# Kernel tuning notes

Measured on AMD Instinct MI355X. Metric: run time of the kernel, lower is better.

Reference implementation:

```python
import jax, jax.numpy as jnp
import numpy as np

N_BATCH = 4096
D_FEAT = 64
N_CLASSES = 10
DET_EPS = 1e-8


def setup_inputs() -> dict:
    key = jax.random.key(0)
    k1, k2, k3 = jax.random.split(key, 3)
    # small-magnitude means and variances bounded away from 0 keep the
    # KL values (and hence sigmoid(KL)) in a numerically meaningful range
    mu = jax.random.normal(k1, (N_BATCH, D_FEAT), dtype=jnp.float32) * 0.1
    var = jax.random.uniform(k2, (N_BATCH, D_FEAT), dtype=jnp.float32) + 0.5
    labels = jax.random.randint(k3, (N_BATCH,), 0, N_CLASSES)
    return {"mu": mu, "var": var, "labels": labels}


def _pairwise_kl(mu, var):
    """K[i, j] = KL(N(mu_i, diag(var_i)) || N(mu_j, diag(var_j))),
    matching the original's kl_mvn on the row/col tiling, but computed
    elementwise/matmul instead of dense diag_embed + inv/det (same math:
    inv(diag(S1)) @ diag(S0) summed == sum(S0/S1); det(diag(S)) == prod(S))."""
    D = mu.shape[1]
    inv_var = 1.0 / var                                   # [N, D]
    # tr term: sum_d var_i,d / var_j,d
    tr = var @ inv_var.T                                  # [N, N]
    # det term: det(S1)/ (det(S0)+eps) with diagonal determinants = products
    p = jnp.prod(var, axis=1)                             # [N]
    det = p[None, :] / (p[:, None] + DET_EPS)             # [N, N]
    # quad term: sum_d (mu_j - mu_i)^2 / var_j,d, expanded into matmuls
    mu_sq = mu * mu                                       # [N, D]
    quad = (mu_sq @ inv_var.T
            - 2.0 * (mu @ (mu * inv_var).T)
            + jnp.sum(mu_sq * inv_var, axis=1)[None, :])  # [N, N]
    return 0.5 * (tr + det + quad - D)


def reference(mu, var, labels):
    N = mu.shape[0]
    K = _pairwise_kl(mu, var)                 # KL(i -> j)
    sym = 0.5 * (K + K.T)                     # symmetric_kl over the pair grid
    logits = jax.nn.sigmoid(sym)              # [N, N]

    same = labels[:, None] == labels[None, :]
    off_diag = ~jnp.eye(N, dtype=bool)        # logits_mask: zero out diagonal
    p_mask = (same & off_diag).astype(logits.dtype)
    n_mask = ((~same) & off_diag).astype(logits.dtype)

    pos = logits * p_mask
    neg = logits * n_mask
    return (jnp.mean(pos), jnp.mean(neg), jnp.sum(pos), jnp.sum(neg))
```

## Files before the change

### kernel.cpp

```cpp
#include <hip/hip_runtime.h>


#define N 4096
#define D 64
#define KH 256
#define MT 128
#define TILES2 32
#define NBLK2 528
#define DET_EPS 1e-8f

typedef short bf16x8 __attribute__((ext_vector_type(8)));
typedef float f32x16 __attribute__((ext_vector_type(16)));

#define WS_H    0
#define WS_PSL  (N * KH * 2)
#define WS_PART (WS_PSL + N * 16)
#define WS_CNT  (WS_PART + 2 * NBLK2 * 4)

static __device__ __forceinline__ unsigned short f2bf(float x) {
  unsigned int u = __float_as_uint(x);
  unsigned int r = (u + 0x7FFFu + ((u >> 16) & 1u)) >> 16;
  return (unsigned short)r;
}

static __device__ __forceinline__ f32x16 mfma_bf16(bf16x8 a, bf16x8 b, f32x16 c) {
  return __builtin_amdgcn_mfma_f32_32x32x16_bf16(a, b, c, 0, 0, 0);
}

__global__ __launch_bounds__(256) void precompute_kernel(
    const float* __restrict__ mu, const float* __restrict__ var,
    const int* __restrict__ labels,
    unsigned short* __restrict__ Hf, float4* __restrict__ PSL,
    int* __restrict__ counter) {
  const int t = threadIdx.x;
  const int lane = t & 63;
  const int w = t >> 6;
  const int r = blockIdx.x * 4 + w;

  if (blockIdx.x == 0 && t == 0) *counter = 0;

  const float m = mu[r * D + lane];
  const float v = var[r * D + lane];
  const float g0 = 1.0f / v;
  const float f0 = v + m * m;
  const float f1 = -2.0f * m;
  const float g1 = m * g0;

  const size_t base = (size_t)(r >> 5) * 8192 + (size_t)(lane >> 2) * 512
                      + (size_t)(r & 31) * 16 + (size_t)(lane & 3) * 4;
  *(ushort4*)&Hf[base] = make_ushort4(f2bf(f0), f2bf(f1), f2bf(g0), f2bf(g1));

  float p = v;
  float s = m * m * g0;
  #pragma unroll
  for (int off = 1; off < 64; off <<= 1) {
    p *= __shfl_xor(p, off);
    s += __shfl_xor(s, off);
  }
  if (lane == 0) {
    PSL[r] = make_float4(p, 1.0f / (p + DET_EPS), 0.25f * s - 16.0f,
                         (float)labels[r]);
  }
}

__global__ __launch_bounds__(256, 2) void pair_kernel(
    const unsigned short* __restrict__ Hf,
    const float4* __restrict__ PSL, float* __restrict__ partial,
    int* __restrict__ counter, float* __restrict__ out) {
  __shared__ float4 sPi[128];
  __shared__ float4 sPj[128];
  __shared__ float red[8];
  __shared__ int lastFlag;
  __shared__ float redp[4], redn[4];

  int L = (int)blockIdx.x;
  int it = (int)(32.5f - sqrtf(32.5f * 32.5f - 2.0f * (float)L));
  while (it > 0 && L < it * TILES2 - it * (it - 1) / 2) --it;
  while (L >= (it + 1) * TILES2 - (it + 1) * it / 2) ++it;
  const int jt = it + (L - (it * TILES2 - it * (it - 1) / 2));
  const int i0 = it * MT, j0 = jt * MT;

  const int t = threadIdx.x;
  const int lane = t & 63;
  const int w = t >> 6;
  const int sr = w >> 1, sc = w & 1;

  if (t < 128) sPi[t] = PSL[i0 + t];
  else sPj[t - 128] = PSL[j0 + t - 128];
  __syncthreads();

  const int l31 = lane & 31;
  const int slot = l31 * 16 + (lane >> 5) * 8;
  const unsigned short* pa = Hf + (size_t)(i0 / 32 + sr * 2) * 8192 + slot;
  const unsigned short* pb = Hf + (size_t)(j0 / 32 + sc * 2) * 8192 + slot;

  const bool active = !(it == jt && w == 2);

  f32x16 C00 = {}, C01 = {}, C10 = {}, C11 = {};
  float pos = 0.0f, neg = 0.0f;

  if (active) {
    #pragma unroll 4
    for (int k = 0; k < 16; ++k) {
      const bf16x8 a0 = *(const bf16x8*)(pa + k * 512);
      const bf16x8 a1 = *(const bf16x8*)(pa + 8192 + k * 512);
      const bf16x8 c0 = *(const bf16x8*)(pb + k * 512);
      const bf16x8 c1 = *(const bf16x8*)(pb + 8192 + k * 512);
      const bf16x8 b0 = __builtin_shufflevector(c0, c0, 2, 3, 0, 1, 6, 7, 4, 5);
      const bf16x8 b1 = __builtin_shufflevector(c1, c1, 2, 3, 0, 1, 6, 7, 4, 5);
      C00 = mfma_bf16(a0, b0, C00);
      C01 = mfma_bf16(a0, b1, C01);
      C10 = mfma_bf16(a1, b0, C10);
      C11 = mfma_bf16(a1, b1, C11);
    }

    const int rbase = 4 * (lane >> 5);
    #pragma unroll
    for (int mn = 0; mn < 4; ++mn) {
      const int m = mn >> 1, n = mn & 1;
      const f32x16 C = (mn == 0) ? C00 : (mn == 1) ? C01 : (mn == 2) ? C10 : C11;
      const int jloc = (sc * 2 + n) * 32 + l31;
      const int j = j0 + jloc;
      const float4 pj = sPj[jloc];
      #pragma unroll
      for (int r = 0; r < 16; ++r) {
        const int row = (r & 3) + 8 * (r >> 2) + rbase;
        const int iloc = (sr * 2 + m) * 32 + row;
        const int i = i0 + iloc;
        if (i < j) {
          const float4 pi = sPi[iloc];
          const float det = pj.x * pi.y + pi.x * pj.y;
          const float sym = 0.25f * (C[r] + det) + pi.z + pj.z;
          const float sig = __builtin_amdgcn_rcpf(1.0f + __expf(-sym));
          if (pi.w == pj.w) pos += sig; else neg += sig;
        }
      }
    }
  }

  #pragma unroll
  for (int off = 32; off > 0; off >>= 1) {
    pos += __shfl_down(pos, off);
    neg += __shfl_down(neg, off);
  }
  if (lane == 0) { red[w] = pos; red[4 + w] = neg; }
  __syncthreads();
  if (t == 0) {
    partial[L]         = red[0] + red[1] + red[2] + red[3];
    partial[NBLK2 + L] = red[4] + red[5] + red[6] + red[7];
    __threadfence();
    const int old = __hip_atomic_fetch_add(counter, 1, __ATOMIC_ACQ_REL,
                                           __HIP_MEMORY_SCOPE_AGENT);
    lastFlag = (old == NBLK2 - 1);
  }
  __syncthreads();

  if (lastFlag) {
    float p = 0.0f, n = 0.0f;
    for (int i = t; i < NBLK2; i += 256) {
      p += __hip_atomic_load(&partial[i], __ATOMIC_RELAXED,
                             __HIP_MEMORY_SCOPE_AGENT);
      n += __hip_atomic_load(&partial[NBLK2 + i], __ATOMIC_RELAXED,
                             __HIP_MEMORY_SCOPE_AGENT);
    }
    #pragma unroll
    for (int off = 32; off > 0; off >>= 1) {
      p += __shfl_down(p, off);
      n += __shfl_down(n, off);
    }
    if (lane == 0) { redp[w] = p; redn[w] = n; }
    __syncthreads();
    if (t == 0) {
      const float posS = 2.0f * (redp[0] + redp[1] + redp[2] + redp[3]);
      const float negS = 2.0f * (redn[0] + redn[1] + redn[2] + redn[3]);
      out[0] = posS * (1.0f / 16777216.0f);
      out[1] = negS * (1.0f / 16777216.0f);
      out[2] = posS;
      out[3] = negS;
    }
  }
}

extern "C" void kernel_launch(void* const* d_in, const int* in_sizes, int n_in,
                              void* d_out, int out_size, void* d_ws, size_t ws_size,
                              hipStream_t stream) {
  const float* mu = (const float*)d_in[0];
  const float* var = (const float*)d_in[1];
  const int* labels = (const int*)d_in[2];
  float* out = (float*)d_out;
  char* ws = (char*)d_ws;

  unsigned short* Hf = (unsigned short*)(ws + WS_H);
  float4* PSL = (float4*)(ws + WS_PSL);
  float* partial = (float*)(ws + WS_PART);
  int* counter = (int*)(ws + WS_CNT);

  precompute_kernel<<<dim3(N / 4), dim3(256), 0, stream>>>(mu, var, labels, Hf,
                                                           PSL, counter);
  pair_kernel<<<dim3(NBLK2), dim3(256), 0, stream>>>(Hf, PSL, partial, counter,
                                                     out);
}
```

Measured before the change: 91.79 us.

## Fuse precompute and pair kernels into one cooperative persistent kernel

Merges the precompute and pairwise kernels into a single cooperative launch of 256 blocks. Grid-wide syncs replace the kernel boundary and the atomic last-block counter. Blocks loop over the 528 triangular tiles in a persistent fashion, and block 0 does the final reduction. This removes one launch plus the atomic handshake, but adds the cost of cooperative launch and grid sync. The tile split is also uneven: some blocks process 3 tiles and others 2.

```diff
diff --git a/kernel.cpp b/kernel.cpp
--- a/kernel.cpp
+++ b/kernel.cpp
@@ -1,4 +1,7 @@
 #include <hip/hip_runtime.h>
+#include <hip/hip_cooperative_groups.h>
+
+namespace cg = cooperative_groups;
 
 
 #define N 4096
@@ -7,6 +10,7 @@
 #define MT 128
 #define TILES2 32
 #define NBLK2 528
+#define GRID 256
 #define DET_EPS 1e-8f
 
 typedef short bf16x8 __attribute__((ext_vector_type(8)));
@@ -15,7 +19,6 @@
 #define WS_H    0
 #define WS_PSL  (N * KH * 2)
 #define WS_PART (WS_PSL + N * 16)
-#define WS_CNT  (WS_PART + 2 * NBLK2 * 4)
 
 static __device__ __forceinline__ unsigned short f2bf(float x) {
   unsigned int u = __float_as_uint(x);
@@ -27,135 +30,132 @@
   return __builtin_amdgcn_mfma_f32_32x32x16_bf16(a, b, c, 0, 0, 0);
 }
 
-__global__ __launch_bounds__(256) void precompute_kernel(
+__global__ __launch_bounds__(256, 2) void fused_kernel(
     const float* __restrict__ mu, const float* __restrict__ var,
     const int* __restrict__ labels,
     unsigned short* __restrict__ Hf, float4* __restrict__ PSL,
-    int* __restrict__ counter) {
+    float* __restrict__ partial, float* __restrict__ out) {
+  cg::grid_group grid = cg::this_grid();
+
+  __shared__ float4 sPi[128];
+  __shared__ float4 sPj[128];
+  __shared__ float red[8];
+  __shared__ float redp[4], redn[4];
+
   const int t = threadIdx.x;
   const int lane = t & 63;
   const int w = t >> 6;
-  const int r = blockIdx.x * 4 + w;
-
-  if (blockIdx.x == 0 && t == 0) *counter = 0;
-
-  const float m = mu[r * D + lane];
-  const float v = var[r * D + lane];
-  const float g0 = 1.0f / v;
-  const float f0 = v + m * m;
-  const float f1 = -2.0f * m;
-  const float g1 = m * g0;
-
-  const size_t base = (size_t)(r >> 5) * 8192 + (size_t)(lane >> 2) * 512
-                      + (size_t)(r & 31) * 16 + (size_t)(lane & 3) * 4;
-  *(ushort4*)&Hf[base] = make_ushort4(f2bf(f0), f2bf(f1), f2bf(g0), f2bf(g1));
-
-  float p = v;
-  float s = m * m * g0;
-  #pragma unroll
-  for (int off = 1; off < 64; off <<= 1) {
-    p *= __shfl_xor(p, off);
-    s += __shfl_xor(s, off);
+
+  {
+    #pragma unroll
+    for (int rep = 0; rep < 4; ++rep) {
+      const int r = (int)blockIdx.x * 16 + rep * 4 + w;
+      const float m = mu[r * D + lane];
+      const float v = var[r * D + lane];
+      const float g0 = 1.0f / v;
+      const float f0 = v + m * m;
+      const float f1 = -2.0f * m;
+      const float g1 = m * g0;
+
+      const size_t base = (size_t)(r >> 5) * 8192 + (size_t)(lane >> 2) * 512
+                          + (size_t)(r & 31) * 16 + (size_t)(lane & 3) * 4;
+      *(ushort4*)&Hf[base] = make_ushort4(f2bf(f0), f2bf(f1), f2bf(g0), f2bf(g1));
+
+      float p = v;
+      float s = m * m * g0;
+      #pragma unroll
+      for (int off = 1; off < 64; off <<= 1) {
+        p *= __shfl_xor(p, off);
+        s += __shfl_xor(s, off);
+      }
+      if (lane == 0) {
+        PSL[r] = make_float4(p, 1.0f / (p + DET_EPS), 0.25f * s - 16.0f,
+                             (float)labels[r]);
+      }
+    }
   }
-  if (lane == 0) {
-    PSL[r] = make_float4(p, 1.0f / (p + DET_EPS), 0.25f * s - 16.0f,
-                         (float)labels[r]);
-  }
-}
-
-__global__ __launch_bounds__(256, 2) void pair_kernel(
-    const unsigned short* __restrict__ Hf,
-    const float4* __restrict__ PSL, float* __restrict__ partial,
-    int* __restrict__ counter, float* __restrict__ out) {
-  __shared__ float4 sPi[128];
-  __shared__ float4 sPj[128];
-  __shared__ float red[8];
-  __shared__ int lastFlag;
-  __shared__ float redp[4], redn[4];
-
-  int L = (int)blockIdx.x;
-  int it = (int)(32.5f - sqrtf(32.5f * 32.5f - 2.0f * (float)L));
-  while (it > 0 && L < it * TILES2 - it * (it - 1) / 2) --it;
-  while (L >= (it + 1) * TILES2 - (it + 1) * it / 2) ++it;
-  const int jt = it + (L - (it * TILES2 - it * (it - 1) / 2));
-  const int i0 = it * MT, j0 = jt * MT;
-
-  const int t = threadIdx.x;
-  const int lane = t & 63;
-  const int w = t >> 6;
+
+  grid.sync();
+
   const int sr = w >> 1, sc = w & 1;
-
-  if (t < 128) sPi[t] = PSL[i0 + t];
-  else sPj[t - 128] = PSL[j0 + t - 128];
-  __syncthreads();
-
   const int l31 = lane & 31;
   const int slot = l31 * 16 + (lane >> 5) * 8;
-  const unsigned short* pa = Hf + (size_t)(i0 / 32 + sr * 2) * 8192 + slot;
-  const unsigned short* pb = Hf + (size_t)(j0 / 32 + sc * 2) * 8192 + slot;
-
-  const bool active = !(it == jt && w == 2);
-
-  f32x16 C00 = {}, C01 = {}, C10 = {}, C11 = {};
-  float pos = 0.0f, neg = 0.0f;
-
-  if (active) {
-    #pragma unroll 4
-    for (int k = 0; k < 16; ++k) {
-      const bf16x8 a0 = *(const bf16x8*)(pa + k * 512);
-      const bf16x8 a1 = *(const bf16x8*)(pa + 8192 + k * 512);
-      const bf16x8 c0 = *(const bf16x8*)(pb + k * 512);
-      const bf16x8 c1 = *(const bf16x8*)(pb + 8192 + k * 512);
-      const bf16x8 b0 = __builtin_shufflevector(c0, c0, 2, 3, 0, 1, 6, 7, 4, 5);
-      const bf16x8 b1 = __builtin_shufflevector(c1, c1, 2, 3, 0, 1, 6, 7, 4, 5);
-      C00 = mfma_bf16(a0, b0, C00);
-      C01 = mfma_bf16(a0, b1, C01);
-      C10 = mfma_bf16(a1, b0, C10);
-      C11 = mfma_bf16(a1, b1, C11);
-    }
-
-    const int rbase = 4 * (lane >> 5);
+
+  for (int L = (int)blockIdx.x; L < NBLK2; L += GRID) {
+    int it = (int)(32.5f - sqrtf(32.5f * 32.5f - 2.0f * (float)L));
+    while (it > 0 && L < it * TILES2 - it * (it - 1) / 2) --it;
+    while (L >= (it + 1) * TILES2 - (it + 1) * it / 2) ++it;
+    const int jt = it + (L - (it * TILES2 - it * (it - 1) / 2));
+    const int i0 = it * MT, j0 = jt * MT;
+
+    __syncthreads();
+    if (t < 128) sPi[t] = PSL[i0 + t];
+    else sPj[t - 128] = PSL[j0 + t - 128];
+    __syncthreads();
+
+    const unsigned short* pa = Hf + (size_t)(i0 / 32 + sr * 2) * 8192 + slot;
+    const unsigned short* pb = Hf + (size_t)(j0 / 32 + sc * 2) * 8192 + slot;
+
+    const bool active = !(it == jt && w == 2);
+
+    f32x16 C00 = {}, C01 = {}, C10 = {}, C11 = {};
+    float pos = 0.0f, neg = 0.0f;
+
+    if (active) {
+      #pragma unroll 4
+      for (int k = 0; k < 16; ++k) {
+        const bf16x8 a0 = *(const bf16x8*)(pa + k * 512);
+        const bf16x8 a1 = *(const bf16x8*)(pa + 8192 + k * 512);
+        const bf16x8 c0 = *(const bf16x8*)(pb + k * 512);
+        const bf16x8 c1 = *(const bf16x8*)(pb + 8192 + k * 512);
+        const bf16x8 b0 = __builtin_shufflevector(c0, c0, 2, 3, 0, 1, 6, 7, 4, 5);
+        const bf16x8 b1 = __builtin_shufflevector(c1, c1, 2, 3, 0, 1, 6, 7, 4, 5);
+        C00 = mfma_bf16(a0, b0, C00);
+        C01 = mfma_bf16(a0, b1, C01);
+        C10 = mfma_bf16(a1, b0, C10);
+        C11 = mfma_bf16(a1, b1, C11);
+      }
+
+      const int rbase = 4 * (lane >> 5);
+      #pragma unroll
+      for (int mn = 0; mn < 4; ++mn) {
+        const int m = mn >> 1, n = mn & 1;
+        const f32x16 C = (mn == 0) ? C00 : (mn == 1) ? C01 : (mn == 2) ? C10 : C11;
+        const int jloc = (sc * 2 + n) * 32 + l31;
+        const int j = j0 + jloc;
+        const float4 pj = sPj[jloc];
+        #pragma unroll
+        for (int r = 0; r < 16; ++r) {
+          const int row = (r & 3) + 8 * (r >> 2) + rbase;
+          const int iloc = (sr * 2 + m) * 32 + row;
+          const int i = i0 + iloc;
+          if (i < j) {
+            const float4 pi = sPi[iloc];
+            const float det = pj.x * pi.y + pi.x * pj.y;
+            const float sym = 0.25f * (C[r] + det) + pi.z + pj.z;
+            const float sig = __builtin_amdgcn_rcpf(1.0f + __expf(-sym));
+            if (pi.w == pj.w) pos += sig; else neg += sig;
+          }
+        }
+      }
+    }
+
     #pragma unroll
-    for (int mn = 0; mn < 4; ++mn) {
-      const int m = mn >> 1, n = mn & 1;
-      const f32x16 C = (mn == 0) ? C00 : (mn == 1) ? C01 : (mn == 2) ? C10 : C11;
-      const int jloc = (sc * 2 + n) * 32 + l31;
-      const int j = j0 + jloc;
-      const float4 pj = sPj[jloc];
-      #pragma unroll
-      for (int r = 0; r < 16; ++r) {
-        const int row = (r & 3) + 8 * (r >> 2) + rbase;
-        const int iloc = (sr * 2 + m) * 32 + row;
-        const int i = i0 + iloc;
-        if (i < j) {
-          const float4 pi = sPi[iloc];
-          const float det = pj.x * pi.y + pi.x * pj.y;
-          const float sym = 0.25f * (C[r] + det) + pi.z + pj.z;
-          const float sig = __builtin_amdgcn_rcpf(1.0f + __expf(-sym));
-          if (pi.w == pj.w) pos += sig; else neg += sig;
-        }
-      }
+    for (int off = 32; off > 0; off >>= 1) {
+      pos += __shfl_down(pos, off);
+      neg += __shfl_down(neg, off);
+    }
+    if (lane == 0) { red[w] = pos; red[4 + w] = neg; }
+    __syncthreads();
+    if (t == 0) {
+      partial[L]         = red[0] + red[1] + red[2] + red[3];
+      partial[NBLK2 + L] = red[4] + red[5] + red[6] + red[7];
     }
   }
 
-  #pragma unroll
-  for (int off = 32; off > 0; off >>= 1) {
-    pos += __shfl_down(pos, off);
-    neg += __shfl_down(neg, off);
-  }
-  if (lane == 0) { red[w] = pos; red[4 + w] = neg; }
-  __syncthreads();
-  if (t == 0) {
-    partial[L]         = red[0] + red[1] + red[2] + red[3];
-    partial[NBLK2 + L] = red[4] + red[5] + red[6] + red[7];
-    __threadfence();
-    const int old = __hip_atomic_fetch_add(counter, 1, __ATOMIC_ACQ_REL,
-                                           __HIP_MEMORY_SCOPE_AGENT);
-    lastFlag = (old == NBLK2 - 1);
-  }
-  __syncthreads();
-
-  if (lastFlag) {
+  grid.sync();
+
+  if (blockIdx.x == 0) {
     float p = 0.0f, n = 0.0f;
     for (int i = t; i < NBLK2; i += 256) {
       p += __hip_atomic_load(&partial[i], __ATOMIC_RELAXED,
@@ -193,10 +193,9 @@
   unsigned short* Hf = (unsigned short*)(ws + WS_H);
   float4* PSL = (float4*)(ws + WS_PSL);
   float* partial = (float*)(ws + WS_PART);
-  int* counter = (int*)(ws + WS_CNT);
-
-  precompute_kernel<<<dim3(N / 4), dim3(256), 0, stream>>>(mu, var, labels, Hf,
-                                                           PSL, counter);
-  pair_kernel<<<dim3(NBLK2), dim3(256), 0, stream>>>(Hf, PSL, partial, counter,
-                                                     out);
-}
+
+  void* args[] = {(void*)&mu, (void*)&var, (void*)&labels,
+                  (void*)&Hf, (void*)&PSL, (void*)&partial, (void*)&out};
+  hipLaunchCooperativeKernel((const void*)fused_kernel, dim3(GRID), dim3(256),
+                             args, 0, stream);
+}
```

New measurement: 154.5 us. 68.3% more time.
